# Performance work log

Hardware: AMD Instinct MI355X
Metric: run time of the kernel (lower is better)

The kernel has to match this reference:

```python
import jax, jax.numpy as jnp
import numpy as np

IN_CH, OUT_CH, HID, NHEAD = 4, 1, 256, 8
VDIM = HID // NHEAD
LOCALITIES = (2.0, 10.0, 10.0, 10.0, 10.0, 200.0)
N_BLOCKS = len(LOCALITIES) - 2
INPUT_RES, LATENT_RES, OUTPUT_RES = (64, 64), (32, 32), (64, 64)
BATCH = 8


def pairwise_dist(res1x, res1y, res2x, res2y):
    gx1 = jnp.linspace(0, 1, res1x + 1)[:-1]
    gy1 = jnp.linspace(0, 1, res1y + 1)[:-1]
    g1x, g1y = jnp.meshgrid(gx1, gy1, indexing='xy')
    grid1 = jnp.stack([g1x.flatten(), g1y.flatten()], axis=-1)
    gx2 = jnp.linspace(0, 1, res2x + 1)[:-1]
    gy2 = jnp.linspace(0, 1, res2y + 1)[:-1]
    g2x, g2y = jnp.meshgrid(gx2, gy2, indexing='xy')
    grid2 = jnp.stack([g2x.flatten(), g2y.flatten()], axis=-1)
    diff = grid1[:, None, :] - grid2[None, :, :]
    return (jnp.sum(diff ** 2, axis=-1) / 2.0).astype(jnp.float32)


def pos_att(m_dist, x, r, w, locality):
    # m_dist:[Nq,Nk]  x:[B,Nk,HID]  r:[H,1,1]  w:[H,HID,VDIM]
    scale = jnp.tan(0.25 * jnp.pi * (1 - 1e-07) * (1 + jnp.sin(r)))
    sd = m_dist[None, :, :] * scale  # [H,Nq,Nk]
    if locality <= 100:
        thr = jnp.percentile(sd, locality, axis=-1, keepdims=True)
        sd = jnp.where(sd <= thr, sd, jnp.inf)
    att = jax.nn.softmax(-sd, axis=-1)  # [H,Nq,Nk]
    value = jnp.einsum('bnj,hjk->bhnk', x, w)  # [B,H,Nk,VDIM]
    out = jnp.einsum('hjn,bhnk->bhjk', att, value)  # [B,H,Nq,VDIM]
    out = jnp.transpose(out, (0, 2, 1, 3)).reshape(x.shape[0], m_dist.shape[0], -1)
    return jax.nn.gelu(out)


def lin(x, w, b):
    # eqx.nn.Linear: w:[out,in], b:[out]
    return jnp.einsum('bni,oi->bno', x, w) + b


def setup_inputs() -> dict:
    key = jax.random.key(0)
    ks = jax.random.split(key, 20)
    Ni = INPUT_RES[0] * INPUT_RES[1]
    s_h = 1.0 / jnp.sqrt(HID)
    s_in = 1.0 / jnp.sqrt(IN_CH)
    return {
        'x': jax.random.normal(ks[0], (BATCH, Ni, IN_CH), jnp.float32),
        'en_fc1_w': jax.random.uniform(ks[1], (HID, IN_CH), jnp.float32, -s_in, s_in),
        'en_fc1_b': jax.random.uniform(ks[2], (HID,), jnp.float32, -s_in, s_in),
        'down_r': jax.random.normal(ks[3], (NHEAD, 1, 1), jnp.float32),
        'down_w': jax.random.normal(ks[4], (NHEAD, HID, VDIM), jnp.float32) * s_h,
        'pa_r': jax.random.normal(ks[5], (N_BLOCKS, NHEAD, 1, 1), jnp.float32),
        'pa_w': jax.random.normal(ks[6], (N_BLOCKS, NHEAD, HID, VDIM), jnp.float32) * s_h,
        'mlp1_w': jax.random.uniform(ks[7], (N_BLOCKS, HID, HID), jnp.float32, -s_h, s_h),
        'mlp1_b': jax.random.uniform(ks[8], (N_BLOCKS, HID), jnp.float32, -s_h, s_h),
        'mlp2_w': jax.random.uniform(ks[9], (N_BLOCKS, HID, HID), jnp.float32, -s_h, s_h),
        'mlp2_b': jax.random.uniform(ks[10], (N_BLOCKS, HID), jnp.float32, -s_h, s_h),
        'res_w': jax.random.uniform(ks[11], (N_BLOCKS, HID, HID), jnp.float32, -s_h, s_h),
        'res_b': jax.random.uniform(ks[12], (N_BLOCKS, HID), jnp.float32, -s_h, s_h),
        'up_r': jax.random.normal(ks[13], (NHEAD, 1, 1), jnp.float32),
        'up_w': jax.random.normal(ks[14], (NHEAD, HID, VDIM), jnp.float32) * s_h,
        'de_fc1_w': jax.random.uniform(ks[15], (HID, HID), jnp.float32, -s_h, s_h),
        'de_fc1_b': jax.random.uniform(ks[16], (HID,), jnp.float32, -s_h, s_h),
        'de_fc2_w': jax.random.uniform(ks[17], (OUT_CH, HID), jnp.float32, -s_h, s_h),
        'de_fc2_b': jax.random.uniform(ks[18], (OUT_CH,), jnp.float32, -s_h, s_h),
    }


def reference(x, en_fc1_w, en_fc1_b, down_r, down_w, pa_r, pa_w,
              mlp1_w, mlp1_b, mlp2_w, mlp2_b, res_w, res_b,
              up_r, up_w, de_fc1_w, de_fc1_b, de_fc2_w, de_fc2_b):
    m_dist_down = pairwise_dist(LATENT_RES[0], LATENT_RES[1], INPUT_RES[0], INPUT_RES[1])
    m_dist_proc = pairwise_dist(LATENT_RES[0], LATENT_RES[1], LATENT_RES[0], LATENT_RES[1])
    m_dist_up = pairwise_dist(OUTPUT_RES[0], OUTPUT_RES[1], LATENT_RES[0], LATENT_RES[1])

    h = jax.nn.gelu(lin(x, en_fc1_w, en_fc1_b))
    h = pos_att(m_dist_down, h, down_r, down_w, LOCALITIES[0])
    for i in range(N_BLOCKS):
        pa_out = pos_att(m_dist_proc, h, pa_r[i], pa_w[i], LOCALITIES[1 + i])
        mlp_out = lin(jax.nn.gelu(lin(pa_out, mlp1_w[i], mlp1_b[i])), mlp2_w[i], mlp2_b[i])
        residual = lin(h, res_w[i], res_b[i])
        h = jax.nn.gelu(mlp_out + residual)
    h = pos_att(m_dist_up, h, up_r, up_w, LOCALITIES[-1])
    h = jax.nn.gelu(lin(h, de_fc1_w, de_fc1_b))
    return lin(h, de_fc2_w, de_fc2_b)
```

## Files before the change

kernel.cpp:

```cpp
#include <hip/hip_runtime.h>
#include <math.h>


#define PI_F 3.14159265358979323846f

typedef __attribute__((ext_vector_type(8))) short short8;
typedef __attribute__((ext_vector_type(4))) float float4v;
typedef __attribute__((ext_vector_type(4))) unsigned short ushort4v;

__device__ __forceinline__ float gelu_f(float x) {
  float u = 0.7978845608028654f * (x + 0.044715f * x * x * x);
  float e = __expf(2.0f * u);
  float t = 1.0f - 2.0f / (e + 1.0f);
  return 0.5f * x * (1.0f + t);
}

__device__ __forceinline__ float head_scale(float r) {
  return tanf(0.25f * PI_F * (1.0f - 1e-7f) * (1.0f + sinf(r)));
}

__device__ __forceinline__ unsigned short f2bf(float f) {
  union { float f; unsigned u; } c; c.f = f;
  unsigned u = c.u + 0x7FFFu + ((c.u >> 16) & 1u);
  return (unsigned short)(u >> 16);
}
__device__ __forceinline__ float bf2f(unsigned short h) {
  union { unsigned u; float f; } c; c.u = ((unsigned)h) << 16;
  return c.f;
}
__device__ __forceinline__ void split_bf(float f, unsigned short& hi,
                                         unsigned short& lo) {
  hi = f2bf(f);
  lo = f2bf(f - bf2f(hi));
}

__global__ __launch_bounds__(256) void k_enc(
    const float* __restrict__ x, const float* __restrict__ w,
    const float* __restrict__ b, unsigned short* __restrict__ ahi,
    unsigned short* __restrict__ alo) {
  int row = blockIdx.x;
  int o = threadIdx.x;
  float4 xv = *(const float4*)(x + (size_t)row * 4);
  float4 wv = *(const float4*)(w + (size_t)o * 4);
  float s = xv.x * wv.x + xv.y * wv.y + xv.z * wv.z + xv.w * wv.w + b[o];
  s = gelu_f(s);
  unsigned short hi, lo;
  split_bf(s, hi, lo);
  ahi[(size_t)row * 256 + o] = hi;
  alo[(size_t)row * 256 + o] = lo;
}

__global__ __launch_bounds__(256) void k_split_all(
    const float* __restrict__ down_w, const float* __restrict__ de1_w,
    const float* __restrict__ up_w, const float* __restrict__ pa_w,
    const float* __restrict__ mlp1_w, const float* __restrict__ mlp2_w,
    const float* __restrict__ res_w, unsigned short* __restrict__ whi,
    unsigned short* __restrict__ wlo) {
  int i = blockIdx.x * 256 + threadIdx.x;
  float f;
  if (i < 65536) {
    int n = i >> 8, k = i & 255;
    f = down_w[(n >> 5) * 8192 + k * 32 + (n & 31)];
  } else if (i < 131072) {
    f = de1_w[i - 65536];
  } else if (i < 196608) {
    int j = i - 131072;
    int n = j >> 8, k = j & 255;
    f = up_w[(n >> 5) * 8192 + k * 32 + (n & 31)];
  } else if (i < 458752) {
    int j = i - 196608;
    int blk = j >> 16, r = j & 65535;
    int n = r >> 8, k = r & 255;
    f = pa_w[(size_t)blk * 65536 + (n >> 5) * 8192 + k * 32 + (n & 31)];
  } else if (i < 720896) {
    f = mlp1_w[i - 458752];
  } else if (i < 983040) {
    f = mlp2_w[i - 720896];
  } else {
    f = res_w[i - 983040];
  }
  unsigned short hi, lo;
  split_bf(f, hi, lo);
  whi[i] = hi;
  wlo[i] = lo;
}

template <int KRES, int CXM, int NPT, int TARGET, int TMAX>
__global__ __launch_bounds__(256) void k_thresh(int* __restrict__ thr) {
  __shared__ int wsum[4];
  int q = blockIdx.x, tid = threadIdx.x;
  int qx = q & 31, qy = q >> 5;
  int cx = qx * CXM, cy = qy * CXM;
  int d[NPT];
#pragma unroll
  for (int j = 0; j < NPT; ++j) {
    int k = tid * NPT + j;
    int kx = k & (KRES - 1), ky = k / KRES;
    int dx = cx - kx, dy = cy - ky;
    d[j] = dx * dx + dy * dy;
  }
  int lo = 0, hi = TMAX;
  while (lo < hi) {
    int mid = (lo + hi) >> 1;
    int c = 0;
#pragma unroll
    for (int j = 0; j < NPT; ++j) c += (d[j] <= mid) ? 1 : 0;
#pragma unroll
    for (int off = 32; off > 0; off >>= 1) c += __shfl_down(c, off, 64);
    if ((tid & 63) == 0) wsum[tid >> 6] = c;
    __syncthreads();
    int total = wsum[0] + wsum[1] + wsum[2] + wsum[3];
    __syncthreads();
    if (total >= TARGET) hi = mid; else lo = mid + 1;
  }
  if (tid == 0) thr[q] = lo;
}

template <int KRES, int CXM, int DSHIFT, int J2>
__global__ __launch_bounds__(256) void k_klist2(
    const float* __restrict__ rvec, const int* __restrict__ thr,
    int* __restrict__ klist2, int* __restrict__ kcnt2,
    float* __restrict__ wlist2) {
  __shared__ int cntS;
  __shared__ int sidx[J2];
  __shared__ int sdv[J2][4];
  __shared__ float denS[8][4];
  int tile = blockIdx.x, tid = threadIdx.x;
  int tx = tile & 15, ty = tile >> 4;
  int cxA[4], cyA[4], T[4];
#pragma unroll
  for (int i = 0; i < 4; ++i) {
    int qx = 2 * tx + (i & 1), qy = 2 * ty + (i >> 1);
    cxA[i] = qx * CXM; cyA[i] = qy * CXM;
    T[i] = thr[qy * 32 + qx];
  }
  if (tid == 0) cntS = 0;
  __syncthreads();
  int x0 = KRES - 1, x1 = 0, y0 = KRES - 1, y1 = 0;
#pragma unroll
  for (int i = 0; i < 4; ++i) {
    int rad = (int)sqrtf((float)T[i]);
    while ((rad + 1) * (rad + 1) <= T[i]) ++rad;
    while (rad > 0 && rad * rad > T[i]) --rad;
    x0 = min(x0, max(0, cxA[i] - rad));
    x1 = max(x1, min(KRES - 1, cxA[i] + rad));
    y0 = min(y0, max(0, cyA[i] - rad));
    y1 = max(y1, min(KRES - 1, cyA[i] + rad));
  }
  int W = x1 - x0 + 1, H = y1 - y0 + 1, tot = W * H;
  for (int p = tid; p < tot; p += 256) {
    int kx = x0 + p % W, ky = y0 + p / W;
    int d[4]; bool keep = false;
#pragma unroll
    for (int i = 0; i < 4; ++i) {
      int dx = cxA[i] - kx, dy = cyA[i] - ky;
      d[i] = dx * dx + dy * dy;
      keep = keep || (d[i] <= T[i]);
    }
    if (keep) {
      int s = atomicAdd(&cntS, 1);
      if (s < J2) {
        sidx[s] = ky * KRES + kx;
#pragma unroll
        for (int i = 0; i < 4; ++i) sdv[s][i] = d[i];
      }
    }
  }
  __syncthreads();
  int cnt = min(cntS, J2);
  int h = tid >> 5, lane = tid & 31;
  float sc = head_scale(rvec[h]) * (1.0f / (float)(1 << DSHIFT));
  float den[4] = {0.f, 0.f, 0.f, 0.f};
  for (int j = lane; j < cnt; j += 32) {
#pragma unroll
    for (int i = 0; i < 4; ++i)
      if (sdv[j][i] <= T[i]) den[i] += __expf(-sc * (float)sdv[j][i]);
  }
#pragma unroll
  for (int i = 0; i < 4; ++i) {
    float d0 = den[i];
#pragma unroll
    for (int off = 16; off > 0; off >>= 1) d0 += __shfl_down(d0, off, 32);
    if (lane == 0) denS[h][i] = d0;
  }
  __syncthreads();
  float inv[4];
#pragma unroll
  for (int i = 0; i < 4; ++i) inv[i] = 1.0f / denS[h][i];
  for (int j = lane; j < cnt; j += 32) {
    float w[4];
#pragma unroll
    for (int i = 0; i < 4; ++i)
      w[i] = (sdv[j][i] <= T[i]) ? __expf(-sc * (float)sdv[j][i]) * inv[i] : 0.f;
    float4v wv = {w[0], w[1], w[2], w[3]};
    *(float4v*)&wlist2[(((size_t)h * 256 + tile) * J2 + j) * 4] = wv;
  }
  if (tid == 0) kcnt2[tile] = cnt;
  if (h == 0)
    for (int j = lane; j < cnt; j += 32) klist2[(size_t)tile * J2 + j] = sidx[j];
}

template <int NK, int J2>
__global__ __launch_bounds__(256) void k_att3(
    const float* __restrict__ value,
    const int* __restrict__ klist2, const int* __restrict__ kcnt2,
    const float* __restrict__ wlist2, unsigned short* __restrict__ ohi,
    unsigned short* __restrict__ olo) {
  __shared__ int kls[J2];
  __shared__ float4v wls[J2];
  __shared__ float4v part[4][4][64];
  int blk = blockIdx.x;
  int tile = blk >> 3, h = blk & 7;
  int tid = threadIdx.x, g = tid & 63, s = tid >> 6;
  int cnt = kcnt2[tile];
  for (int j = tid; j < cnt; j += 256) {
    kls[j] = klist2[(size_t)tile * J2 + j];
    wls[j] = *(const float4v*)&wlist2[(((size_t)h * 256 + tile) * J2 + j) * 4];
  }
  __syncthreads();
  const float* vb = value + (size_t)h * NK * 256 + g * 4;
  float4v acc[4];
#pragma unroll
  for (int i = 0; i < 4; ++i) acc[i] = (float4v)0.0f;
  for (int j = s; j < cnt; j += 4) {
    int row = kls[j];
    float4v v = *(const float4v*)(vb + (size_t)row * 256);
    float4v w = wls[j];
    acc[0] += w.x * v;
    acc[1] += w.y * v;
    acc[2] += w.z * v;
    acc[3] += w.w * v;
  }
#pragma unroll
  for (int i = 0; i < 4; ++i) part[s][i][g] = acc[i];
  __syncthreads();
  if (tid < 64) {
    int g2 = tid;
    int ttx = tile & 15, tty = tile >> 4;
    int batch = g2 >> 3, v0 = (g2 & 7) * 4;
#pragma unroll
    for (int i = 0; i < 4; ++i) {
      float4v o4 = part[0][i][g2] + part[1][i][g2] + part[2][i][g2] +
                   part[3][i][g2];
      int q = (2 * tty + (i >> 1)) * 32 + 2 * ttx + (i & 1);
      size_t idx = ((size_t)batch * 1024 + q) * 256 + h * 32 + v0;
      ushort4v hv, lv;
#pragma unroll
      for (int c = 0; c < 4; ++c) {
        float oo = gelu_f(o4[c]);
        unsigned short hi, lo;
        split_bf(oo, hi, lo);
        hv[c] = hi; lv[c] = lo;
      }
      *(ushort4v*)(ohi + idx) = hv;
      *(ushort4v*)(olo + idx) = lv;
    }
  }
}

template <bool DUAL, int OL, bool GEL, bool OHILO>
__global__ __launch_bounds__(256) void k_mf(
    const unsigned short* __restrict__ A1hi, const unsigned short* __restrict__ A1lo,
    const unsigned short* __restrict__ W1hi, const unsigned short* __restrict__ W1lo,
    const unsigned short* __restrict__ A2hi, const unsigned short* __restrict__ A2lo,
    const unsigned short* __restrict__ W2hi, const unsigned short* __restrict__ W2lo,
    const float* __restrict__ bias, const float* __restrict__ bias2,
    float* __restrict__ outf, unsigned short* __restrict__ ohi,
    unsigned short* __restrict__ olo, int NS) {
  __shared__ unsigned short Ah[128][40], Al[128][40];
  __shared__ unsigned short Bh[128][40], Bl[128][40];
  int tid = threadIdx.x;
  int m0 = blockIdx.x * 128, n0 = blockIdx.y * 128;
  int w = tid >> 6, lane = tid & 63;
  int wm = (w >> 1) * 64, wn = (w & 1) * 64;
  int quad = lane >> 4, l16 = lane & 15;
  float4v acc[4][4];
#pragma unroll
  for (int i = 0; i < 4; ++i)
#pragma unroll
    for (int j = 0; j < 4; ++j) acc[i][j] = (float4v)0.0f;

  int srow = tid >> 1, skq = (tid & 1) * 16;
  const int KT = DUAL ? 512 : 256;
  for (int kk = 0; kk < KT; kk += 32) {
    const unsigned short *pAh, *pAl, *pWh, *pWl;
    int kb;
    if (DUAL && kk >= 256) {
      pAh = A2hi; pAl = A2lo; pWh = W2hi; pWl = W2lo; kb = kk - 256;
    } else {
      pAh = A1hi; pAl = A1lo; pWh = W1hi; pWl = W1lo; kb = kk;
    }
    {
      size_t ga = (size_t)(m0 + srow) * 256 + kb + skq;
      const uint4* pah = (const uint4*)(pAh + ga);
      const uint4* pal = (const uint4*)(pAl + ga);
      *(uint4*)&Ah[srow][skq] = pah[0];
      *(uint4*)&Ah[srow][skq + 8] = pah[1];
      *(uint4*)&Al[srow][skq] = pal[0];
      *(uint4*)&Al[srow][skq + 8] = pal[1];
      size_t gb = (size_t)(n0 + srow) * 256 + kb + skq;
      const uint4* pbh = (const uint4*)(pWh + gb);
      const uint4* pbl = (const uint4*)(pWl + gb);
      *(uint4*)&Bh[srow][skq] = pbh[0];
      *(uint4*)&Bh[srow][skq + 8] = pbh[1];
      *(uint4*)&Bl[srow][skq] = pbl[0];
      *(uint4*)&Bl[srow][skq + 8] = pbl[1];
    }
    __syncthreads();
    short8 ah[4], al[4], bh[4], bl[4];
#pragma unroll
    for (int s = 0; s < 4; ++s) {
      ah[s] = *(const short8*)&Ah[wm + s * 16 + l16][quad * 8];
      al[s] = *(const short8*)&Al[wm + s * 16 + l16][quad * 8];
      bh[s] = *(const short8*)&Bh[wn + s * 16 + l16][quad * 8];
      bl[s] = *(const short8*)&Bl[wn + s * 16 + l16][quad * 8];
    }
#pragma unroll
    for (int ms = 0; ms < 4; ++ms)
#pragma unroll
      for (int ns = 0; ns < 4; ++ns) {
        acc[ms][ns] = __builtin_amdgcn_mfma_f32_16x16x32_bf16(
            ah[ms], bh[ns], acc[ms][ns], 0, 0, 0);
        acc[ms][ns] = __builtin_amdgcn_mfma_f32_16x16x32_bf16(
            ah[ms], bl[ns], acc[ms][ns], 0, 0, 0);
        acc[ms][ns] = __builtin_amdgcn_mfma_f32_16x16x32_bf16(
            al[ms], bh[ns], acc[ms][ns], 0, 0, 0);
      }
    __syncthreads();
  }
#pragma unroll
  for (int ms = 0; ms < 4; ++ms) {
#pragma unroll
    for (int ns = 0; ns < 4; ++ns) {
      int n = n0 + wn + ns * 16 + l16;
      float bv = bias ? bias[n] : 0.0f;
      if (DUAL && bias2) bv += bias2[n];
#pragma unroll
      for (int r = 0; r < 4; ++r) {
        int m = m0 + wm + ms * 16 + quad * 4 + r;
        float c = acc[ms][ns][r] + bv;
        if (GEL) c = gelu_f(c);
        if (OHILO) {
          unsigned short chi, clo;
          split_bf(c, chi, clo);
          ohi[(size_t)m * 256 + n] = chi;
          olo[(size_t)m * 256 + n] = clo;
        } else if (OL == 0) {
          outf[(size_t)m * 256 + n] = c;
        } else {
          int N = 1 << NS;
          int bb = m >> NS, rr = m & (N - 1);
          outf[(((size_t)(n >> 5) * N + rr) * 8 + bb) * 32 + (n & 31)] = c;
        }
      }
    }
  }
}

template <bool DUAL, int OL, bool GEL, bool OHILO>
__global__ __launch_bounds__(256) void k_mf2(
    const unsigned short* __restrict__ A1hi, const unsigned short* __restrict__ A1lo,
    const unsigned short* __restrict__ W1hi, const unsigned short* __restrict__ W1lo,
    const unsigned short* __restrict__ A2hi, const unsigned short* __restrict__ A2lo,
    const unsigned short* __restrict__ W2hi, const unsigned short* __restrict__ W2lo,
    const float* __restrict__ bias, const float* __restrict__ bias2,
    float* __restrict__ outf, unsigned short* __restrict__ ohi,
    unsigned short* __restrict__ olo, int NS) {
  __shared__ unsigned short Ah[64][40], Al[64][40];
  __shared__ unsigned short Bh[64][40], Bl[64][40];
  int tid = threadIdx.x;
  int m0 = blockIdx.x * 64, n0 = blockIdx.y * 64;
  int w = tid >> 6, lane = tid & 63;
  int wm = (w >> 1) * 32, wn = (w & 1) * 32;
  int quad = lane >> 4, l16 = lane & 15;
  float4v acc[2][2];
#pragma unroll
  for (int i = 0; i < 2; ++i)
#pragma unroll
    for (int j = 0; j < 2; ++j) acc[i][j] = (float4v)0.0f;

  int srow = tid >> 2, skq = (tid & 3) * 8;
  const int KT = DUAL ? 512 : 256;
  for (int kk = 0; kk < KT; kk += 32) {
    const unsigned short *pAh, *pAl, *pWh, *pWl;
    int kb;
    if (DUAL && kk >= 256) {
      pAh = A2hi; pAl = A2lo; pWh = W2hi; pWl = W2lo; kb = kk - 256;
    } else {
      pAh = A1hi; pAl = A1lo; pWh = W1hi; pWl = W1lo; kb = kk;
    }
    {
      size_t ga = (size_t)(m0 + srow) * 256 + kb + skq;
      *(uint4*)&Ah[srow][skq] = *(const uint4*)(pAh + ga);
      *(uint4*)&Al[srow][skq] = *(const uint4*)(pAl + ga);
      size_t gb = (size_t)(n0 + srow) * 256 + kb + skq;
      *(uint4*)&Bh[srow][skq] = *(const uint4*)(pWh + gb);
      *(uint4*)&Bl[srow][skq] = *(const uint4*)(pWl + gb);
    }
    __syncthreads();
    short8 ah[2], al[2], bh[2], bl[2];
#pragma unroll
    for (int s = 0; s < 2; ++s) {
      ah[s] = *(const short8*)&Ah[wm + s * 16 + l16][quad * 8];
      al[s] = *(const short8*)&Al[wm + s * 16 + l16][quad * 8];
      bh[s] = *(const short8*)&Bh[wn + s * 16 + l16][quad * 8];
      bl[s] = *(const short8*)&Bl[wn + s * 16 + l16][quad * 8];
    }
#pragma unroll
    for (int ms = 0; ms < 2; ++ms)
#pragma unroll
      for (int ns = 0; ns < 2; ++ns) {
        acc[ms][ns] = __builtin_amdgcn_mfma_f32_16x16x32_bf16(
            ah[ms], bh[ns], acc[ms][ns], 0, 0, 0);
        acc[ms][ns] = __builtin_amdgcn_mfma_f32_16x16x32_bf16(
            ah[ms], bl[ns], acc[ms][ns], 0, 0, 0);
        acc[ms][ns] = __builtin_amdgcn_mfma_f32_16x16x32_bf16(
            al[ms], bh[ns], acc[ms][ns], 0, 0, 0);
      }
    __syncthreads();
  }
#pragma unroll
  for (int ms = 0; ms < 2; ++ms) {
#pragma unroll
    for (int ns = 0; ns < 2; ++ns) {
      int n = n0 + wn + ns * 16 + l16;
      float bv = bias ? bias[n] : 0.0f;
      if (DUAL && bias2) bv += bias2[n];
#pragma unroll
      for (int r = 0; r < 4; ++r) {
        int m = m0 + wm + ms * 16 + quad * 4 + r;
        float c = acc[ms][ns][r] + bv;
        if (GEL) c = gelu_f(c);
        if (OHILO) {
          unsigned short chi, clo;
          split_bf(c, chi, clo);
          ohi[(size_t)m * 256 + n] = chi;
          olo[(size_t)m * 256 + n] = clo;
        } else if (OL == 0) {
          outf[(size_t)m * 256 + n] = c;
        } else {
          int N = 1 << NS;
          int bb = m >> NS, rr = m & (N - 1);
          outf[(((size_t)(n >> 5) * N + rr) * 8 + bb) * 32 + (n & 31)] = c;
        }
      }
    }
  }
}

__global__ __launch_bounds__(256) void k_up_s1(
    const float* __restrict__ value,
    const float* __restrict__ rvec, float* __restrict__ T) {
  __shared__ float AxL[64][33];
  int ky = blockIdx.x, h = blockIdx.y, tid = threadIdx.x;
  float sc = head_scale(rvec[h]) * (1.0f / 8192.0f);
  float v[32];
  const float* vb = value + ((size_t)h * 1024 + ky * 32) * 256 + tid;
#pragma unroll
  for (int kx = 0; kx < 32; ++kx) v[kx] = vb[kx * 256];
  if (tid < 64) {
    int qx = tid, dxmin = qx & 1;
    for (int kx = 0; kx < 32; ++kx) {
      int dx = qx - 2 * kx;
      AxL[qx][kx] = __expf(-sc * (float)(dx * dx - dxmin));
    }
  }
  __syncthreads();
  float* tb = T + (((size_t)h * 64) * 32 + ky) * 256 + tid;
  for (int qx = 0; qx < 64; ++qx) {
    float acc = 0.f;
#pragma unroll
    for (int kx = 0; kx < 32; ++kx) acc += AxL[qx][kx] * v[kx];
    tb[(size_t)qx * 32 * 256] = acc;
  }
}

__global__ __launch_bounds__(256) void k_up_s2(
    const float* __restrict__ T, const float* __restrict__ rvec,
    unsigned short* __restrict__ ohi, unsigned short* __restrict__ olo) {
  __shared__ float AyL[64][33];
  __shared__ float Sy[64];
  __shared__ float SxS;
  int qx = blockIdx.x, h = blockIdx.y, tid = threadIdx.x;
  float sc = head_scale(rvec[h]) * (1.0f / 8192.0f);
  float t[32];
  const float* tb = T + ((size_t)h * 64 + qx) * 32 * 256 + tid;
#pragma unroll
  for (int ky = 0; ky < 32; ++ky) t[ky] = tb[ky * 256];
  if (tid < 64) {
    int qy = tid, dymin = qy & 1;
    float s = 0.f;
    for (int ky = 0; ky < 32; ++ky) {
      int dy = qy - 2 * ky;
      float e = __expf(-sc * (float)(dy * dy - dymin));
      AyL[qy][ky] = e;
      s += e;
    }
    Sy[qy] = s;
  } else if (tid >= 64 && tid < 96) {
    int kx = tid - 64, dxmin = qx & 1;
    int dx = qx - 2 * kx;
    float e = __expf(-sc * (float)(dx * dx - dxmin));
#pragma unroll
    for (int off = 16; off > 0; off >>= 1) e += __shfl_down(e, off, 32);
    if (kx == 0) SxS = e;
  }
  __syncthreads();
  float invSx = 1.0f / SxS;
  int b = tid >> 5, v = tid & 31;
  size_t base = ((size_t)b * 4096 + qx) * 256 + h * 32 + v;
  for (int qy = 0; qy < 64; ++qy) {
    float acc = 0.f;
#pragma unroll
    for (int ky = 0; ky < 32; ++ky) acc += AyL[qy][ky] * t[ky];
    float o = gelu_f(acc * invSx / Sy[qy]);
    unsigned short hi, lo;
    split_bf(o, hi, lo);
    size_t idx = base + (size_t)qy * 64 * 256;
    ohi[idx] = hi;
    olo[idx] = lo;
  }
}

__global__ __launch_bounds__(256) void k_fc2(const float* __restrict__ h,
                                             const float* __restrict__ w,
                                             const float* __restrict__ b,
                                             float* __restrict__ out) {
  int row = blockIdx.x * 4 + (threadIdx.x >> 6);
  int lane = threadIdx.x & 63;
  float4 hv = *(const float4*)(h + (size_t)row * 256 + lane * 4);
  float4 wv = *(const float4*)(w + lane * 4);
  float s = hv.x * wv.x + hv.y * wv.y + hv.z * wv.z + hv.w * wv.w;
#pragma unroll
  for (int off = 32; off > 0; off >>= 1) s += __shfl_down(s, off, 64);
  if (lane == 0) out[row] = s + b[0];
}

extern "C" void kernel_launch(void* const* d_in, const int* in_sizes, int n_in,
                              void* d_out, int out_size, void* d_ws,
                              size_t ws_size, hipStream_t stream) {
  const float* x      = (const float*)d_in[0];
  const float* en_w   = (const float*)d_in[1];
  const float* en_b   = (const float*)d_in[2];
  const float* down_r = (const float*)d_in[3];
  const float* down_w = (const float*)d_in[4];
  const float* pa_r   = (const float*)d_in[5];
  const float* pa_w   = (const float*)d_in[6];
  const float* mlp1_w = (const float*)d_in[7];
  const float* mlp1_b = (const float*)d_in[8];
  const float* mlp2_w = (const float*)d_in[9];
  const float* mlp2_b = (const float*)d_in[10];
  const float* res_w  = (const float*)d_in[11];
  const float* res_b  = (const float*)d_in[12];
  const float* up_r   = (const float*)d_in[13];
  const float* up_w   = (const float*)d_in[14];
  const float* de1_w  = (const float*)d_in[15];
  const float* de1_b  = (const float*)d_in[16];
  const float* de2_w  = (const float*)d_in[17];
  const float* de2_b  = (const float*)d_in[18];
  float* out = (float*)d_out;

  constexpr int J2 = 256;
  float* ws = (float*)d_ws;
  unsigned short* Ahi = (unsigned short*)ws;
  unsigned short* Alo = Ahi + 8388608;
  float* B = ws + 8388608;
  float* Tbuf = B + 2097152;
  unsigned short* hAhi = (unsigned short*)(ws + 16777216);
  unsigned short* hAlo = hAhi + 2097152;
  unsigned short* hBhi = hAlo + 2097152;
  unsigned short* hBlo = hBhi + 2097152;
  unsigned short* pahi = hBlo + 2097152;
  unsigned short* palo = pahi + 2097152;
  unsigned short* m1hi = palo + 2097152;
  unsigned short* m1lo = m1hi + 2097152;
  int* thrD = (int*)(ws + 25165824);
  int* thrP = thrD + 1024;
  int* cntD2 = thrP + 1024;
  int* cntP2 = cntD2 + 256;
  int* klD2 = cntP2 + 256;
  int* klP2 = klD2 + 256 * J2;
  float* wlD2 = (float*)(klP2 + 256 * J2);
  float* wlP2 = wlD2 + 2097152;
  unsigned short* Whi = (unsigned short*)(wlP2 + 2097152);
  unsigned short* Wlo = Whi + 1245184;
  const int WO_DOWN = 0, WO_DE1 = 65536, WO_UP = 131072, WO_PA = 196608,
            WO_MLP1 = 458752, WO_MLP2 = 720896, WO_RES = 983040;

  k_enc<<<32768, 256, 0, stream>>>(x, en_w, en_b, Ahi, Alo);
  k_split_all<<<4864, 256, 0, stream>>>(down_w, de1_w, up_w, pa_w, mlp1_w,
                                        mlp2_w, res_w, Whi, Wlo);
  k_thresh<64, 2, 16, 82, 7938><<<1024, 256, 0, stream>>>(thrD);
  k_thresh<32, 1, 4, 103, 1922><<<1024, 256, 0, stream>>>(thrP);
  k_klist2<64, 2, 13, J2><<<256, 256, 0, stream>>>(down_r, thrD, klD2, cntD2,
                                                   wlD2);
  k_klist2<32, 1, 11, J2><<<256, 256, 0, stream>>>(pa_r, thrP, klP2, cntP2,
                                                   wlP2);
  k_mf<false, 1, false, false><<<dim3(256, 2), 256, 0, stream>>>(
      Ahi, Alo, Whi + WO_DOWN, Wlo + WO_DOWN, nullptr, nullptr, nullptr,
      nullptr, nullptr, nullptr, B, nullptr, nullptr, 12);
  k_att3<4096, J2><<<2048, 256, 0, stream>>>(B, klD2, cntD2, wlD2, hAhi, hAlo);
  for (int i = 0; i < 4; ++i) {
    const unsigned short* hih = (i & 1) ? hBhi : hAhi;
    const unsigned short* hil = (i & 1) ? hBlo : hAlo;
    unsigned short* hoh = (i & 1) ? hAhi : hBhi;
    unsigned short* hol = (i & 1) ? hAlo : hBlo;
    k_mf2<false, 1, false, false><<<dim3(128, 4), 256, 0, stream>>>(
        hih, hil, Whi + WO_PA + i * 65536, Wlo + WO_PA + i * 65536, nullptr,
        nullptr, nullptr, nullptr, nullptr, nullptr, B, nullptr, nullptr, 10);
    k_att3<1024, J2><<<2048, 256, 0, stream>>>(B, klP2, cntP2, wlP2, pahi,
                                               palo);
    k_mf2<false, 0, true, true><<<dim3(128, 4), 256, 0, stream>>>(
        pahi, palo, Whi + WO_MLP1 + i * 65536, Wlo + WO_MLP1 + i * 65536,
        nullptr, nullptr, nullptr, nullptr, mlp1_b + i * 256, nullptr, nullptr,
        m1hi, m1lo, 0);
    k_mf2<true, 0, true, true><<<dim3(128, 4), 256, 0, stream>>>(
        m1hi, m1lo, Whi + WO_MLP2 + i * 65536, Wlo + WO_MLP2 + i * 65536, hih,
        hil, Whi + WO_RES + i * 65536, Wlo + WO_RES + i * 65536,
        mlp2_b + i * 256, res_b + i * 256, nullptr, hoh, hol, 0);
  }
  k_mf2<false, 1, false, false><<<dim3(128, 4), 256, 0, stream>>>(
      hAhi, hAlo, Whi + WO_UP, Wlo + WO_UP, nullptr, nullptr, nullptr, nullptr,
      nullptr, nullptr, B, nullptr, nullptr, 10);
  k_up_s1<<<dim3(32, 8), 256, 0, stream>>>(B, up_r, Tbuf);
  k_up_s2<<<dim3(64, 8), 256, 0, stream>>>(Tbuf, up_r, Ahi, Alo);
  k_mf<false, 0, true, false><<<dim3(256, 2), 256, 0, stream>>>(
      Ahi, Alo, Whi + WO_DE1, Wlo + WO_DE1, nullptr, nullptr, nullptr, nullptr,
      de1_b, nullptr, B, nullptr, nullptr, 0);
  k_fc2<<<8192, 256, 0, stream>>>(B, de2_w, de2_b, out);
}
```

Measured before the change: 490.2 us.

## Replace GEMM kernels with full-K weight staging and direct-register A loads

The two split-bf16 GEMM kernels are merged into one templated kernel. Each block now stages a 32-column weight slab covering all of K in shared memory once, and streams A fragments from global memory straight into registers with one-step prefetch, so the per-K-tile shared-memory staging and barriers go away. The block index is remapped so that 8 consecutive blocks share m-rows across N tiles, aiming for L2 reuse of A. The trade-off is that A is read once per 32-column N tile (8 times per row) with no shared-memory reuse, and tiles are narrower.

```diff
diff --git a/kernel.cpp b/kernel.cpp
--- a/kernel.cpp
+++ b/kernel.cpp
@@ -258,8 +258,8 @@
   }
 }
 
-template <bool DUAL, int OL, bool GEL, bool OHILO>
-__global__ __launch_bounds__(256) void k_mf(
+template <int MS, bool DUAL, int OL, bool GEL, bool OHILO>
+__global__ __launch_bounds__(256) void k_gemm(
     const unsigned short* __restrict__ A1hi, const unsigned short* __restrict__ A1lo,
     const unsigned short* __restrict__ W1hi, const unsigned short* __restrict__ W1lo,
     const unsigned short* __restrict__ A2hi, const unsigned short* __restrict__ A2lo,
@@ -267,168 +267,98 @@
     const float* __restrict__ bias, const float* __restrict__ bias2,
     float* __restrict__ outf, unsigned short* __restrict__ ohi,
     unsigned short* __restrict__ olo, int NS) {
-  __shared__ unsigned short Ah[128][40], Al[128][40];
-  __shared__ unsigned short Bh[128][40], Bl[128][40];
+  constexpr int MT = MS * 64;
+  __shared__ alignas(16) unsigned short Bh[32][264];
+  __shared__ alignas(16) unsigned short Bl[32][264];
   int tid = threadIdx.x;
-  int m0 = blockIdx.x * 128, n0 = blockIdx.y * 128;
+  int b = blockIdx.x;
+  int per = gridDim.x >> 3;
+  int mpx = per >> 3;
+  int x = b & 7, j = b >> 3;
+  int m0 = (x * mpx + (j >> 3)) * MT;
+  int n0 = (j & 7) * 32;
   int w = tid >> 6, lane = tid & 63;
-  int wm = (w >> 1) * 64, wn = (w & 1) * 64;
   int quad = lane >> 4, l16 = lane & 15;
-  float4v acc[4][4];
-#pragma unroll
-  for (int i = 0; i < 4; ++i)
-#pragma unroll
-    for (int j = 0; j < 4; ++j) acc[i][j] = (float4v)0.0f;
-
-  int srow = tid >> 1, skq = (tid & 1) * 16;
-  const int KT = DUAL ? 512 : 256;
-  for (int kk = 0; kk < KT; kk += 32) {
-    const unsigned short *pAh, *pAl, *pWh, *pWl;
-    int kb;
-    if (DUAL && kk >= 256) {
-      pAh = A2hi; pAl = A2lo; pWh = W2hi; pWl = W2lo; kb = kk - 256;
-    } else {
-      pAh = A1hi; pAl = A1lo; pWh = W1hi; pWl = W1lo; kb = kk;
-    }
+
+  float4v acc[MS][2];
+#pragma unroll
+  for (int i = 0; i < MS; ++i)
+#pragma unroll
+    for (int n = 0; n < 2; ++n) acc[i][n] = (float4v)0.0f;
+
+  const int NPASS = DUAL ? 2 : 1;
+  for (int p = 0; p < NPASS; ++p) {
+    const unsigned short* pAh = p ? A2hi : A1hi;
+    const unsigned short* pAl = p ? A2lo : A1lo;
+    const unsigned short* pWh = p ? W2hi : W1hi;
+    const unsigned short* pWl = p ? W2lo : W1lo;
+    __syncthreads();
     {
-      size_t ga = (size_t)(m0 + srow) * 256 + kb + skq;
-      const uint4* pah = (const uint4*)(pAh + ga);
-      const uint4* pal = (const uint4*)(pAl + ga);
-      *(uint4*)&Ah[srow][skq] = pah[0];
-      *(uint4*)&Ah[srow][skq + 8] = pah[1];
-      *(uint4*)&Al[srow][skq] = pal[0];
-      *(uint4*)&Al[srow][skq + 8] = pal[1];
-      size_t gb = (size_t)(n0 + srow) * 256 + kb + skq;
-      const uint4* pbh = (const uint4*)(pWh + gb);
-      const uint4* pbl = (const uint4*)(pWl + gb);
-      *(uint4*)&Bh[srow][skq] = pbh[0];
-      *(uint4*)&Bh[srow][skq + 8] = pbh[1];
-      *(uint4*)&Bl[srow][skq] = pbl[0];
-      *(uint4*)&Bl[srow][skq + 8] = pbl[1];
+      int row = tid >> 3, seg = (tid & 7) * 32;
+      const uint4* gh = (const uint4*)(pWh + (size_t)(n0 + row) * 256 + seg);
+      const uint4* gl = (const uint4*)(pWl + (size_t)(n0 + row) * 256 + seg);
+#pragma unroll
+      for (int q = 0; q < 4; ++q) {
+        *(uint4*)&Bh[row][seg + q * 8] = gh[q];
+        *(uint4*)&Bl[row][seg + q * 8] = gl[q];
+      }
     }
     __syncthreads();
-    short8 ah[4], al[4], bh[4], bl[4];
-#pragma unroll
-    for (int s = 0; s < 4; ++s) {
-      ah[s] = *(const short8*)&Ah[wm + s * 16 + l16][quad * 8];
-      al[s] = *(const short8*)&Al[wm + s * 16 + l16][quad * 8];
-      bh[s] = *(const short8*)&Bh[wn + s * 16 + l16][quad * 8];
-      bl[s] = *(const short8*)&Bl[wn + s * 16 + l16][quad * 8];
-    }
-#pragma unroll
-    for (int ms = 0; ms < 4; ++ms)
-#pragma unroll
-      for (int ns = 0; ns < 4; ++ns) {
-        acc[ms][ns] = __builtin_amdgcn_mfma_f32_16x16x32_bf16(
-            ah[ms], bh[ns], acc[ms][ns], 0, 0, 0);
-        acc[ms][ns] = __builtin_amdgcn_mfma_f32_16x16x32_bf16(
-            ah[ms], bl[ns], acc[ms][ns], 0, 0, 0);
-        acc[ms][ns] = __builtin_amdgcn_mfma_f32_16x16x32_bf16(
-            al[ms], bh[ns], acc[ms][ns], 0, 0, 0);
+    const unsigned short* ah_p[MS];
+    const unsigned short* al_p[MS];
+#pragma unroll
+    for (int ms = 0; ms < MS; ++ms) {
+      size_t row = (size_t)(m0 + w * MS * 16 + ms * 16 + l16);
+      ah_p[ms] = pAh + row * 256 + quad * 8;
+      al_p[ms] = pAl + row * 256 + quad * 8;
+    }
+    short8 nah[MS], nal[MS];
+#pragma unroll
+    for (int ms = 0; ms < MS; ++ms) {
+      nah[ms] = *(const short8*)(ah_p[ms]);
+      nal[ms] = *(const short8*)(al_p[ms]);
+    }
+#pragma unroll
+    for (int ks = 0; ks < 8; ++ks) {
+      short8 cah[MS], cal[MS];
+#pragma unroll
+      for (int ms = 0; ms < MS; ++ms) { cah[ms] = nah[ms]; cal[ms] = nal[ms]; }
+      if (ks < 7) {
+#pragma unroll
+        for (int ms = 0; ms < MS; ++ms) {
+          nah[ms] = *(const short8*)(ah_p[ms] + (ks + 1) * 32);
+          nal[ms] = *(const short8*)(al_p[ms] + (ks + 1) * 32);
+        }
       }
-    __syncthreads();
-  }
-#pragma unroll
-  for (int ms = 0; ms < 4; ++ms) {
-#pragma unroll
-    for (int ns = 0; ns < 4; ++ns) {
-      int n = n0 + wn + ns * 16 + l16;
+      short8 bh[2], bl[2];
+#pragma unroll
+      for (int ns = 0; ns < 2; ++ns) {
+        bh[ns] = *(const short8*)&Bh[ns * 16 + l16][ks * 32 + quad * 8];
+        bl[ns] = *(const short8*)&Bl[ns * 16 + l16][ks * 32 + quad * 8];
+      }
+#pragma unroll
+      for (int ms = 0; ms < MS; ++ms)
+#pragma unroll
+        for (int ns = 0; ns < 2; ++ns) {
+          acc[ms][ns] = __builtin_amdgcn_mfma_f32_16x16x32_bf16(
+              cah[ms], bh[ns], acc[ms][ns], 0, 0, 0);
+          acc[ms][ns] = __builtin_amdgcn_mfma_f32_16x16x32_bf16(
+              cah[ms], bl[ns], acc[ms][ns], 0, 0, 0);
+          acc[ms][ns] = __builtin_amdgcn_mfma_f32_16x16x32_bf16(
+              cal[ms], bh[ns], acc[ms][ns], 0, 0, 0);
+        }
+    }
+  }
+#pragma unroll
+  for (int ms = 0; ms < MS; ++ms) {
+#pragma unroll
+    for (int ns = 0; ns < 2; ++ns) {
+      int n = n0 + ns * 16 + l16;
       float bv = bias ? bias[n] : 0.0f;
       if (DUAL && bias2) bv += bias2[n];
 #pragma unroll
       for (int r = 0; r < 4; ++r) {
-        int m = m0 + wm + ms * 16 + quad * 4 + r;
-        float c = acc[ms][ns][r] + bv;
-        if (GEL) c = gelu_f(c);
-        if (OHILO) {
-          unsigned short chi, clo;
-          split_bf(c, chi, clo);
-          ohi[(size_t)m * 256 + n] = chi;
-          olo[(size_t)m * 256 + n] = clo;
-        } else if (OL == 0) {
-          outf[(size_t)m * 256 + n] = c;
-        } else {
-          int N = 1 << NS;
-          int bb = m >> NS, rr = m & (N - 1);
-          outf[(((size_t)(n >> 5) * N + rr) * 8 + bb) * 32 + (n & 31)] = c;
-        }
-      }
-    }
-  }
-}
-
-template <bool DUAL, int OL, bool GEL, bool OHILO>
-__global__ __launch_bounds__(256) void k_mf2(
-    const unsigned short* __restrict__ A1hi, const unsigned short* __restrict__ A1lo,
-    const unsigned short* __restrict__ W1hi, const unsigned short* __restrict__ W1lo,
-    const unsigned short* __restrict__ A2hi, const unsigned short* __restrict__ A2lo,
-    const unsigned short* __restrict__ W2hi, const unsigned short* __restrict__ W2lo,
-    const float* __restrict__ bias, const float* __restrict__ bias2,
-    float* __restrict__ outf, unsigned short* __restrict__ ohi,
-    unsigned short* __restrict__ olo, int NS) {
-  __shared__ unsigned short Ah[64][40], Al[64][40];
-  __shared__ unsigned short Bh[64][40], Bl[64][40];
-  int tid = threadIdx.x;
-  int m0 = blockIdx.x * 64, n0 = blockIdx.y * 64;
-  int w = tid >> 6, lane = tid & 63;
-  int wm = (w >> 1) * 32, wn = (w & 1) * 32;
-  int quad = lane >> 4, l16 = lane & 15;
-  float4v acc[2][2];
-#pragma unroll
-  for (int i = 0; i < 2; ++i)
-#pragma unroll
-    for (int j = 0; j < 2; ++j) acc[i][j] = (float4v)0.0f;
-
-  int srow = tid >> 2, skq = (tid & 3) * 8;
-  const int KT = DUAL ? 512 : 256;
-  for (int kk = 0; kk < KT; kk += 32) {
-    const unsigned short *pAh, *pAl, *pWh, *pWl;
-    int kb;
-    if (DUAL && kk >= 256) {
-      pAh = A2hi; pAl = A2lo; pWh = W2hi; pWl = W2lo; kb = kk - 256;
-    } else {
-      pAh = A1hi; pAl = A1lo; pWh = W1hi; pWl = W1lo; kb = kk;
-    }
-    {
-      size_t ga = (size_t)(m0 + srow) * 256 + kb + skq;
-      *(uint4*)&Ah[srow][skq] = *(const uint4*)(pAh + ga);
-      *(uint4*)&Al[srow][skq] = *(const uint4*)(pAl + ga);
-      size_t gb = (size_t)(n0 + srow) * 256 + kb + skq;
-      *(uint4*)&Bh[srow][skq] = *(const uint4*)(pWh + gb);
-      *(uint4*)&Bl[srow][skq] = *(const uint4*)(pWl + gb);
-    }
-    __syncthreads();
-    short8 ah[2], al[2], bh[2], bl[2];
-#pragma unroll
-    for (int s = 0; s < 2; ++s) {
-      ah[s] = *(const short8*)&Ah[wm + s * 16 + l16][quad * 8];
-      al[s] = *(const short8*)&Al[wm + s * 16 + l16][quad * 8];
-      bh[s] = *(const short8*)&Bh[wn + s * 16 + l16][quad * 8];
-      bl[s] = *(const short8*)&Bl[wn + s * 16 + l16][quad * 8];
-    }
-#pragma unroll
-    for (int ms = 0; ms < 2; ++ms)
-#pragma unroll
-      for (int ns = 0; ns < 2; ++ns) {
-        acc[ms][ns] = __builtin_amdgcn_mfma_f32_16x16x32_bf16(
-            ah[ms], bh[ns], acc[ms][ns], 0, 0, 0);
-        acc[ms][ns] = __builtin_amdgcn_mfma_f32_16x16x32_bf16(
-            ah[ms], bl[ns], acc[ms][ns], 0, 0, 0);
-        acc[ms][ns] = __builtin_amdgcn_mfma_f32_16x16x32_bf16(
-            al[ms], bh[ns], acc[ms][ns], 0, 0, 0);
-      }
-    __syncthreads();
-  }
-#pragma unroll
-  for (int ms = 0; ms < 2; ++ms) {
-#pragma unroll
-    for (int ns = 0; ns < 2; ++ns) {
-      int n = n0 + wn + ns * 16 + l16;
-      float bv = bias ? bias[n] : 0.0f;
-      if (DUAL && bias2) bv += bias2[n];
-#pragma unroll
-      for (int r = 0; r < 4; ++r) {
-        int m = m0 + wm + ms * 16 + quad * 4 + r;
+        int m = m0 + w * MS * 16 + ms * 16 + quad * 4 + r;
         float c = acc[ms][ns][r] + bv;
         if (GEL) c = gelu_f(c);
         if (OHILO) {
@@ -596,7 +526,7 @@
                                                    wlD2);
   k_klist2<32, 1, 11, J2><<<256, 256, 0, stream>>>(pa_r, thrP, klP2, cntP2,
                                                    wlP2);
-  k_mf<false, 1, false, false><<<dim3(256, 2), 256, 0, stream>>>(
+  k_gemm<4, false, 1, false, false><<<1024, 256, 0, stream>>>(
       Ahi, Alo, Whi + WO_DOWN, Wlo + WO_DOWN, nullptr, nullptr, nullptr,
       nullptr, nullptr, nullptr, B, nullptr, nullptr, 12);
   k_att3<4096, J2><<<2048, 256, 0, stream>>>(B, klD2, cntD2, wlD2, hAhi, hAlo);
@@ -605,26 +535,26 @@
     const unsigned short* hil = (i & 1) ? hBlo : hAlo;
     unsigned short* hoh = (i & 1) ? hAhi : hBhi;
     unsigned short* hol = (i & 1) ? hAlo : hBlo;
-    k_mf2<false, 1, false, false><<<dim3(128, 4), 256, 0, stream>>>(
+    k_gemm<2, false, 1, false, false><<<512, 256, 0, stream>>>(
         hih, hil, Whi + WO_PA + i * 65536, Wlo + WO_PA + i * 65536, nullptr,
         nullptr, nullptr, nullptr, nullptr, nullptr, B, nullptr, nullptr, 10);
     k_att3<1024, J2><<<2048, 256, 0, stream>>>(B, klP2, cntP2, wlP2, pahi,
                                                palo);
-    k_mf2<false, 0, true, true><<<dim3(128, 4), 256, 0, stream>>>(
+    k_gemm<2, false, 0, true, true><<<512, 256, 0, stream>>>(
         pahi, palo, Whi + WO_MLP1 + i * 65536, Wlo + WO_MLP1 + i * 65536,
         nullptr, nullptr, nullptr, nullptr, mlp1_b + i * 256, nullptr, nullptr,
         m1hi, m1lo, 0);
-    k_mf2<true, 0, true, true><<<dim3(128, 4), 256, 0, stream>>>(
+    k_gemm<2, true, 0, true, true><<<512, 256, 0, stream>>>(
         m1hi, m1lo, Whi + WO_MLP2 + i * 65536, Wlo + WO_MLP2 + i * 65536, hih,
         hil, Whi + WO_RES + i * 65536, Wlo + WO_RES + i * 65536,
         mlp2_b + i * 256, res_b + i * 256, nullptr, hoh, hol, 0);
   }
-  k_mf2<false, 1, false, false><<<dim3(128, 4), 256, 0, stream>>>(
+  k_gemm<2, false, 1, false, false><<<512, 256, 0, stream>>>(
       hAhi, hAlo, Whi + WO_UP, Wlo + WO_UP, nullptr, nullptr, nullptr, nullptr,
       nullptr, nullptr, B, nullptr, nullptr, 10);
   k_up_s1<<<dim3(32, 8), 256, 0, stream>>>(B, up_r, Tbuf);
   k_up_s2<<<dim3(64, 8), 256, 0, stream>>>(Tbuf, up_r, Ahi, Alo);
-  k_mf<false, 0, true, false><<<dim3(256, 2), 256, 0, stream>>>(
+  k_gemm<4, false, 0, true, false><<<1024, 256, 0, stream>>>(
       Ahi, Alo, Whi + WO_DE1, Wlo + WO_DE1, nullptr, nullptr, nullptr, nullptr,
       de1_b, nullptr, B, nullptr, nullptr, 0);
   k_fc2<<<8192, 256, 0, stream>>>(B, de2_w, de2_b, out);
```

Result: slower. 560.5 us (+14.3%).
